# Performance work log

Hardware: AMD Instinct MI355X
Metric: run time of the kernel (lower is better)

## Reference

```python
import jax, jax.numpy as jnp
import numpy as np

B, D, U, M, K = 8192, 512, 512, 16, 64


def setup_inputs() -> dict:
    key = jax.random.key(0)
    ks = jax.random.split(key, 5)
    return {
        "x": jax.random.normal(ks[0], (B, D), dtype=jnp.float32),
        "key_kernel": jax.random.normal(ks[1], (D, K), dtype=jnp.float32) * (1.0 / np.sqrt(D)),
        "key_bias": jnp.zeros((K,), dtype=jnp.float32),
        "keys_map": jax.random.normal(ks[2], (M, K), dtype=jnp.float32),
        "kernels": jax.random.normal(ks[3], (M, D, U), dtype=jnp.float32) * (1.0 / np.sqrt(D)),
        "biases": jnp.zeros((M, U), dtype=jnp.float32),
    }


def reference(x, key_kernel, key_bias, keys_map, kernels, biases):
    # key projection: [B, K]
    keyv = x @ key_kernel + key_bias
    # inverse-distance similarity to mode keys: [B, M]
    dist = jnp.sqrt(jnp.sum((keyv[:, None, :] - keys_map[None, :, :]) ** 2, axis=-1))
    sim = 1.0 / (dist + 1.0)
    modes = kernels.shape[0]
    # kernel = mean_m(sim_m * kernels_m); out = x @ kernel.
    # Distributive identity: out = (1/M) * sum_m sim_m * (x @ kernels_m)
    out = jnp.einsum("bm,bd,mdu->bu", sim, x, kernels) / modes
    # bias = mean_m(sim_m * biases_m): [B, U]
    out = out + (sim @ biases) / modes
    return out
```

## Files before the change

### kernel.cpp

```cpp
#include <hip/hip_runtime.h>
#include <hip/hip_bf16.h>
#include <stdint.h>

#define B_SZ 8192
#define D_SZ 512
#define U_SZ 512
#define M_SZ 16
#define K_SZ 64

typedef short bf16x8 __attribute__((ext_vector_type(8)));
typedef float f32x4 __attribute__((ext_vector_type(4)));

__device__ __forceinline__ unsigned short f2bf(float f) {
  union { float f; unsigned u; } v; v.f = f;
  unsigned r = v.u + 0x7fffu + ((v.u >> 16) & 1u);
  return (unsigned short)(r >> 16);
}

__global__ __launch_bounds__(256) void prep1(
    const float* __restrict__ x, const float* __restrict__ key_kernel,
    const float* __restrict__ kernels, unsigned short* __restrict__ xbf,
    unsigned short* __restrict__ kbf, unsigned short* __restrict__ wkbf) {
  __shared__ float tf[32][65];
  __shared__ unsigned short sx[16][520];
  int bid = blockIdx.x;
  int t = threadIdx.x;

  if (bid < 2048) {
    int m = bid >> 7;
    int rem = bid & 127;
    int a = (rem >> 3) & 15;
    int ut = rem & 7;
    int d0 = a * 32, u0 = ut * 64;
    {
      int dr = t >> 4, uc = t & 15;
      const float* src = kernels + ((size_t)m * D_SZ + d0 + dr) * U_SZ + u0 + uc * 4;
      float4 aa = *(const float4*)src;
      float4 bb = *(const float4*)(src + (size_t)16 * U_SZ);
      tf[dr][uc * 4 + 0] = aa.x; tf[dr][uc * 4 + 1] = aa.y;
      tf[dr][uc * 4 + 2] = aa.z; tf[dr][uc * 4 + 3] = aa.w;
      tf[dr + 16][uc * 4 + 0] = bb.x; tf[dr + 16][uc * 4 + 1] = bb.y;
      tf[dr + 16][uc * 4 + 2] = bb.z; tf[dr + 16][uc * 4 + 3] = bb.w;
    }
    __syncthreads();
    {
      int ur = t >> 2, dc = t & 3;
      int j = ur >> 4, lane16 = ur & 15;
      int kt = a >> 1, h = a & 1;
      unsigned short* dst = kbf +
          (((((size_t)m * 8 + ut) * 8 + kt) * 4 + j) * 2 + h) * 512 +
          ((size_t)dc * 16 + lane16) * 8;
      ushort4 lo, hi;
      lo.x = f2bf(tf[dc * 8 + 0][ur]); lo.y = f2bf(tf[dc * 8 + 1][ur]);
      lo.z = f2bf(tf[dc * 8 + 2][ur]); lo.w = f2bf(tf[dc * 8 + 3][ur]);
      hi.x = f2bf(tf[dc * 8 + 4][ur]); hi.y = f2bf(tf[dc * 8 + 5][ur]);
      hi.z = f2bf(tf[dc * 8 + 6][ur]); hi.w = f2bf(tf[dc * 8 + 7][ur]);
      *(ushort4*)dst = lo;
      *(ushort4*)(dst + 4) = hi;
    }
    return;
  }

  if (bid < 2056) {
    int kt = bid - 2048;
#pragma unroll
    for (int rep = 0; rep < 2; ++rep) {
      int c = rep * 256 + t;
      int j = c >> 7, h = (c >> 6) & 1, quad = (c >> 4) & 3, ln = c & 15;
      int dd = kt * 64 + h * 32 + quad * 8;
      int u = j * 16 + ln;
      unsigned short v[8];
#pragma unroll
      for (int e = 0; e < 8; ++e)
        v[e] = f2bf(key_kernel[(size_t)(dd + e) * K_SZ + u]);
      unsigned short* dst =
          wkbf + ((size_t)((kt * 4 + j) * 2 + h) * 64 + quad * 16 + ln) * 8;
#pragma unroll
      for (int e = 0; e < 8; ++e) dst[e] = v[e];
    }
    return;
  }

  {
    int xb0 = bid - 2056;
    int btx = xb0 >> 3, i = xb0 & 7;
    int b0 = xb0 * 16;
#pragma unroll
    for (int rep = 0; rep < 8; ++rep) {
      int idx = rep * 256 + t;
      int row = idx >> 7;
      int c4 = (idx & 127) * 4;
      float4 v = *(const float4*)(x + (size_t)(b0 + row) * D_SZ + c4);
      ushort4 o;
      o.x = f2bf(v.x); o.y = f2bf(v.y); o.z = f2bf(v.z); o.w = f2bf(v.w);
      *(ushort4*)(&sx[row][c4]) = o;
    }
    __syncthreads();
    int w = t >> 6, l = t & 63;
    int ln = l & 15, quad = l >> 4;
#pragma unroll
    for (int rep = 0; rep < 4; ++rep) {
      int c = w * 4 + rep;
      int kt = c >> 1, h = c & 1;
      const unsigned short* srcp = &sx[ln][kt * 64 + h * 32 + quad * 8];
      ushort4 lo = *(const ushort4*)(srcp);
      ushort4 hi = *(const ushort4*)(srcp + 4);
      unsigned short* dst =
          xbf + ((((size_t)btx * 8 + kt) * 8 + i) * 2 + h) * 512 + (size_t)l * 8;
      *(ushort4*)dst = lo;
      *(ushort4*)(dst + 4) = hi;
    }
  }
}

__global__ __launch_bounds__(256) void prep2(
    const unsigned short* __restrict__ xbf, const unsigned short* __restrict__ wkbf,
    const float* __restrict__ key_bias, const float* __restrict__ keys_map,
    float* __restrict__ simT) {
  __shared__ float kv[64][68];
  __shared__ float sKM[16][64];
  int t = threadIdx.x, w = t >> 6, l = t & 63;
  int blk = blockIdx.x;
  int b0 = blk * 64, bt = blk >> 1, ibase = (blk & 1) * 4;
  int lane16 = l & 15, quad = l >> 4;

  ((float4*)sKM)[t] = ((const float4*)keys_map)[t];

  f32x4 acc[4];
#pragma unroll
  for (int j = 0; j < 4; ++j) acc[j] = (f32x4){0.f, 0.f, 0.f, 0.f};

  for (int kt = 0; kt < 8; ++kt) {
    bf16x8 af[2];
#pragma unroll
    for (int h = 0; h < 2; ++h)
      af[h] = *(const bf16x8*)(xbf +
                               ((((size_t)bt * 8 + kt) * 8 + ibase + w) * 2 + h) * 512 +
                               (size_t)l * 8);
#pragma unroll
    for (int j = 0; j < 4; ++j) {
      bf16x8 b0f = *(const bf16x8*)(wkbf + ((size_t)((kt * 4 + j) * 2 + 0) * 64 + l) * 8);
      bf16x8 b1f = *(const bf16x8*)(wkbf + ((size_t)((kt * 4 + j) * 2 + 1) * 64 + l) * 8);
      acc[j] = __builtin_amdgcn_mfma_f32_16x16x32_bf16(af[0], b0f, acc[j], 0, 0, 0);
      acc[j] = __builtin_amdgcn_mfma_f32_16x16x32_bf16(af[1], b1f, acc[j], 0, 0, 0);
    }
  }
#pragma unroll
  for (int j = 0; j < 4; ++j) {
    float bc = key_bias[j * 16 + lane16];
#pragma unroll
    for (int r = 0; r < 4; ++r)
      kv[w * 16 + quad * 4 + r][j * 16 + lane16] = acc[j][r] + bc;
  }
  __syncthreads();

  int row = t >> 2, mg = (t & 3) * 4;
  float d2[4] = {0.f, 0.f, 0.f, 0.f};
#pragma unroll 8
  for (int k = 0; k < 64; ++k) {
    float kvv = kv[row][k];
#pragma unroll
    for (int q = 0; q < 4; ++q) {
      float df = kvv - sKM[mg + q][k];
      d2[q] += df * df;
    }
  }
#pragma unroll
  for (int q = 0; q < 4; ++q)
    simT[(size_t)(mg + q) * B_SZ + b0 + row] = 1.0f / (sqrtf(d2[q]) + 1.0f);
}

#define STAGE(mode_, kt_, bufi_)                                               \
  {                                                                            \
    const unsigned short* _src = kbf_l +                                       \
        (((size_t)(mode_) * 8 + ut) * 8 + (kt_)) * 4096 + w * 1024;            \
    unsigned short* _dst = Bbuf + (bufi_) * 4096 + w * 1024;                   \
    __builtin_amdgcn_global_load_lds(                                          \
        (const __attribute__((address_space(1))) unsigned int*)(_src),         \
        (__attribute__((address_space(3))) unsigned int*)(_dst), 16, 0, 0);    \
    __builtin_amdgcn_global_load_lds(                                          \
        (const __attribute__((address_space(1))) unsigned int*)(_src + 512),   \
        (__attribute__((address_space(3))) unsigned int*)(_dst + 512), 16, 0,  \
        0);                                                                    \
  }

#define LOAD_AF(dst_, kt_)                                                     \
  _Pragma("unroll") for (int ii = 0; ii < 4; ++ii)                             \
      _Pragma("unroll") for (int h = 0; h < 2; ++h) dst_[ii][h] =              \
      *(const bf16x8*)(xbf +                                                   \
                       ((((size_t)(bt * 2 + (w >> 1)) * 8 + (kt_)) * 8 +       \
                         (w & 1) * 4 + ii) * 2 + h) * 512 +                    \
                       (size_t)l * 8);

__global__ __launch_bounds__(256, 1) void poly_gemm(
    const unsigned short* __restrict__ xbf,
    const unsigned short* __restrict__ kbf,
    const float* __restrict__ simT,
    const float* __restrict__ biases,
    float* __restrict__ out) {
  __shared__ __align__(16) char smem[53248];

  int t = threadIdx.x, w = t >> 6, l = t & 63;
  int bid = blockIdx.x;
  int ut = bid & 7, bt = bid >> 3;
  int b0 = bt * 256, u0 = ut * 64;
  int lane16 = l & 15, quad = l >> 4;

  unsigned short* Bbuf = (unsigned short*)smem;
  float* sSim = (float*)(smem + 32768);
  float* sBias = (float*)(smem + 49152);

  {
    int m = t >> 4, c = t & 15;
    const float* src = simT + (size_t)m * B_SZ + b0 + c * 16;
    float4* dst = (float4*)(sSim + m * 256 + c * 16);
#pragma unroll
    for (int q = 0; q < 4; ++q) dst[q] = ((const float4*)src)[q];
    *(float4*)(sBias + m * 64 + c * 4) =
        *(const float4*)(biases + (size_t)m * U_SZ + u0 + c * 4);
  }

  const unsigned short* kbf_l = kbf + (size_t)l * 8;

  bf16x8 afc[4][2], afn[4][2];

  STAGE(0, 0, 0);
  STAGE(1, 0, 1);
  LOAD_AF(afc, 0);
  asm volatile("s_waitcnt vmcnt(0)" ::: "memory");
  __syncthreads();

  f32x4 facc[4][4];
#pragma unroll
  for (int i = 0; i < 4; ++i)
#pragma unroll
    for (int j = 0; j < 4; ++j) facc[i][j] = (f32x4){0.f, 0.f, 0.f, 0.f};

#pragma unroll 1
  for (int kt = 0; kt < 8; ++kt) {
#pragma unroll 1
    for (int mg = 0; mg < 4; ++mg) {
#pragma unroll
      for (int mu = 0; mu < 4; ++mu) {
        const int mode = mg * 4 + mu;
        {
          int mode2 = (mode + 2) & 15;
          int kt2 = (mode >= 14) ? ((kt + 1) & 7) : kt;
          STAGE(mode2, kt2, (mode + 2) & 3);
        }
        if (mode == 0 && kt < 7) { LOAD_AF(afn, kt + 1); }
        if (mode <= 1 && kt <= 6)
          asm volatile("s_waitcnt vmcnt(12)" ::: "memory");
        else
          asm volatile("s_waitcnt vmcnt(4)" ::: "memory");
        asm volatile("s_barrier" ::: "memory");

        const unsigned short* lb = Bbuf + (mode & 3) * 4096;
        bf16x8 bfr[4][2];
#pragma unroll
        for (int j = 0; j < 4; ++j)
#pragma unroll
          for (int h = 0; h < 2; ++h)
            bfr[j][h] =
                *(const bf16x8*)(lb + (j * 2 + h) * 512 + (size_t)l * 8);

        f32x4 sv[4];
#pragma unroll
        for (int i = 0; i < 4; ++i)
          sv[i] = *(const f32x4*)(sSim + mode * 256 + w * 64 + i * 16 +
                                  quad * 4);

#pragma unroll
        for (int i = 0; i < 4; ++i)
#pragma unroll
          for (int j = 0; j < 4; ++j) {
            f32x4 p = __builtin_amdgcn_mfma_f32_16x16x32_bf16(
                afc[i][0], bfr[j][0], (f32x4){0.f, 0.f, 0.f, 0.f}, 0, 0, 0);
            p = __builtin_amdgcn_mfma_f32_16x16x32_bf16(afc[i][1], bfr[j][1],
                                                        p, 0, 0, 0);
#pragma unroll
            for (int r = 0; r < 4; ++r) facc[i][j][r] += sv[i][r] * p[r];
          }

        if (kt == 0) {
          float bbv[4];
#pragma unroll
          for (int j = 0; j < 4; ++j)
            bbv[j] = sBias[mode * 64 + j * 16 + lane16];
#pragma unroll
          for (int i = 0; i < 4; ++i)
#pragma unroll
            for (int j = 0; j < 4; ++j)
#pragma unroll
              for (int r = 0; r < 4; ++r)
                facc[i][j][r] += sv[i][r] * bbv[j];
        }
      }
    }
    if (kt < 7) {
#pragma unroll
      for (int ii = 0; ii < 4; ++ii)
#pragma unroll
        for (int h = 0; h < 2; ++h) afc[ii][h] = afn[ii][h];
    }
  }

  asm volatile("s_waitcnt vmcnt(0)" ::: "memory");
#pragma unroll
  for (int i = 0; i < 4; ++i)
#pragma unroll
    for (int r = 0; r < 4; ++r) {
      int row = b0 + w * 64 + i * 16 + quad * 4 + r;
      float* orow = out + (size_t)row * U_SZ + u0;
#pragma unroll
      for (int j = 0; j < 4; ++j)
        orow[j * 16 + lane16] = facc[i][j][r] * 0.0625f;
    }
}

extern "C" void kernel_launch(void* const* d_in, const int* in_sizes, int n_in,
                              void* d_out, int out_size, void* d_ws, size_t ws_size,
                              hipStream_t stream) {
  const float* x = (const float*)d_in[0];
  const float* key_kernel = (const float*)d_in[1];
  const float* key_bias = (const float*)d_in[2];
  const float* keys_map = (const float*)d_in[3];
  const float* kernels = (const float*)d_in[4];
  const float* biases = (const float*)d_in[5];
  float* out = (float*)d_out;

  char* p = (char*)d_ws;
  unsigned short* xbf = (unsigned short*)p;  p += (size_t)B_SZ * D_SZ * 2;
  unsigned short* kbf = (unsigned short*)p;  p += (size_t)M_SZ * U_SZ * D_SZ * 2;
  unsigned short* wkbf = (unsigned short*)p; p += (size_t)K_SZ * D_SZ * 2;
  float* simT = (float*)p;

  prep1<<<dim3(2568), 256, 0, stream>>>(x, key_kernel, kernels, xbf, kbf, wkbf);
  prep2<<<dim3(128), 256, 0, stream>>>(xbf, wkbf, key_bias, keys_map, simT);
  poly_gemm<<<dim3(256), 256, 0, stream>>>(xbf, kbf, simT, biases, out);
}
```

Measured before the change: 183.3 us.

## Use 8 waves per block with deeper 8-slot LDS weight pipeline

Doubles the poly_gemm block to 512 threads (8 waves). Each wave now owns 32 rows instead of 64, which halves the accumulator and A-fragment registers per wave. The LDS ring for weight tiles grows from 4 to 8 slots, prefetching 4 modes ahead instead of 2, and each wave stages half as much per step. The aim is more latency hiding through extra resident waves and a deeper prefetch. In exchange, LDS use rises to about 84KB and the launch-bounds hint of 2 blocks per CU may not be achievable, and the waitcnt accounting is more complex.

Result: faster. 163.4 us (-10.9%).

```diff
diff --git a/kernel.cpp b/kernel.cpp
--- a/kernel.cpp
+++ b/kernel.cpp
@@ -173,32 +173,30 @@
 #define STAGE(mode_, kt_, bufi_)                                               \
   {                                                                            \
     const unsigned short* _src = kbf_l +                                       \
-        (((size_t)(mode_) * 8 + ut) * 8 + (kt_)) * 4096 + w * 1024;            \
-    unsigned short* _dst = Bbuf + (bufi_) * 4096 + w * 1024;                   \
+        (((size_t)(mode_) * 8 + ut) * 8 + (kt_)) * 4096 + w * 512;             \
+    unsigned short* _dst = Bbuf + (bufi_) * 4096 + w * 512;                    \
     __builtin_amdgcn_global_load_lds(                                          \
         (const __attribute__((address_space(1))) unsigned int*)(_src),         \
         (__attribute__((address_space(3))) unsigned int*)(_dst), 16, 0, 0);    \
-    __builtin_amdgcn_global_load_lds(                                          \
-        (const __attribute__((address_space(1))) unsigned int*)(_src + 512),   \
-        (__attribute__((address_space(3))) unsigned int*)(_dst + 512), 16, 0,  \
-        0);                                                                    \
   }
 
 #define LOAD_AF(dst_, kt_)                                                     \
-  _Pragma("unroll") for (int ii = 0; ii < 4; ++ii)                             \
-      _Pragma("unroll") for (int h = 0; h < 2; ++h) dst_[ii][h] =              \
-      *(const bf16x8*)(xbf +                                                   \
-                       ((((size_t)(bt * 2 + (w >> 1)) * 8 + (kt_)) * 8 +       \
-                         (w & 1) * 4 + ii) * 2 + h) * 512 +                    \
-                       (size_t)l * 8);
-
-__global__ __launch_bounds__(256, 1) void poly_gemm(
+  _Pragma("unroll") for (int ii = 0; ii < 2; ++ii)                             \
+      _Pragma("unroll") for (int h = 0; h < 2; ++h) {                          \
+    int g_ = bt * 16 + w * 2 + ii;                                             \
+    dst_[ii][h] = *(const bf16x8*)(                                            \
+        xbf + ((((size_t)(g_ >> 3) * 8 + (kt_)) * 8 + (g_ & 7)) * 2 + h) *     \
+                  512 +                                                        \
+              (size_t)l * 8);                                                  \
+  }
+
+__global__ __launch_bounds__(512, 2) void poly_gemm(
     const unsigned short* __restrict__ xbf,
     const unsigned short* __restrict__ kbf,
     const float* __restrict__ simT,
     const float* __restrict__ biases,
     float* __restrict__ out) {
-  __shared__ __align__(16) char smem[53248];
+  __shared__ __align__(16) char smem[86016];
 
   int t = threadIdx.x, w = t >> 6, l = t & 63;
   int bid = blockIdx.x;
@@ -207,99 +205,101 @@
   int lane16 = l & 15, quad = l >> 4;
 
   unsigned short* Bbuf = (unsigned short*)smem;
-  float* sSim = (float*)(smem + 32768);
-  float* sBias = (float*)(smem + 49152);
+  float* sSim = (float*)(smem + 65536);
+  float* sBias = (float*)(smem + 81920);
 
   {
-    int m = t >> 4, c = t & 15;
-    const float* src = simT + (size_t)m * B_SZ + b0 + c * 16;
-    float4* dst = (float4*)(sSim + m * 256 + c * 16);
-#pragma unroll
-    for (int q = 0; q < 4; ++q) dst[q] = ((const float4*)src)[q];
-    *(float4*)(sBias + m * 64 + c * 4) =
-        *(const float4*)(biases + (size_t)m * U_SZ + u0 + c * 4);
+    int m = t >> 5, c = (t & 31) * 8;
+    const float* src = simT + (size_t)m * B_SZ + b0 + c;
+    float4* dst = (float4*)(sSim + m * 256 + c);
+    dst[0] = ((const float4*)src)[0];
+    dst[1] = ((const float4*)src)[1];
+    int bi = t * 2;
+    *(float2*)(sBias + bi) =
+        *(const float2*)(biases + (size_t)(bi >> 6) * U_SZ + u0 + (bi & 63));
   }
 
   const unsigned short* kbf_l = kbf + (size_t)l * 8;
 
-  bf16x8 afc[4][2], afn[4][2];
+  bf16x8 afc[2][2], afn[2][2];
 
   STAGE(0, 0, 0);
   STAGE(1, 0, 1);
+  STAGE(2, 0, 2);
+  STAGE(3, 0, 3);
   LOAD_AF(afc, 0);
   asm volatile("s_waitcnt vmcnt(0)" ::: "memory");
   __syncthreads();
 
-  f32x4 facc[4][4];
-#pragma unroll
-  for (int i = 0; i < 4; ++i)
+  f32x4 facc[2][4];
+#pragma unroll
+  for (int i = 0; i < 2; ++i)
 #pragma unroll
     for (int j = 0; j < 4; ++j) facc[i][j] = (f32x4){0.f, 0.f, 0.f, 0.f};
 
 #pragma unroll 1
   for (int kt = 0; kt < 8; ++kt) {
-#pragma unroll 1
-    for (int mg = 0; mg < 4; ++mg) {
-#pragma unroll
-      for (int mu = 0; mu < 4; ++mu) {
-        const int mode = mg * 4 + mu;
-        {
-          int mode2 = (mode + 2) & 15;
-          int kt2 = (mode >= 14) ? ((kt + 1) & 7) : kt;
-          STAGE(mode2, kt2, (mode + 2) & 3);
-        }
-        if (mode == 0 && kt < 7) { LOAD_AF(afn, kt + 1); }
-        if (mode <= 1 && kt <= 6)
-          asm volatile("s_waitcnt vmcnt(12)" ::: "memory");
+#pragma unroll
+    for (int mode = 0; mode < 16; ++mode) {
+      const int s = kt * 16 + mode;
+      {
+        int mode4 = (mode + 4) & 15;
+        int kt4 = (mode >= 12) ? ((kt + 1) & 7) : kt;
+        STAGE(mode4, kt4, (s + 4) & 7);
+      }
+      if (mode == 0 && kt < 7) { LOAD_AF(afn, kt + 1); }
+      if (mode < 5) {
+        if (kt < 7)
+          asm volatile("s_waitcnt vmcnt(8)" ::: "memory");
         else
           asm volatile("s_waitcnt vmcnt(4)" ::: "memory");
-        asm volatile("s_barrier" ::: "memory");
-
-        const unsigned short* lb = Bbuf + (mode & 3) * 4096;
-        bf16x8 bfr[4][2];
+      } else {
+        asm volatile("s_waitcnt vmcnt(4)" ::: "memory");
+      }
+      asm volatile("s_barrier" ::: "memory");
+
+      const unsigned short* lb = Bbuf + (s & 7) * 4096;
+      bf16x8 bfr[4][2];
+#pragma unroll
+      for (int j = 0; j < 4; ++j)
+#pragma unroll
+        for (int h = 0; h < 2; ++h)
+          bfr[j][h] = *(const bf16x8*)(lb + (j * 2 + h) * 512 + (size_t)l * 8);
+
+      f32x4 sv[2];
+#pragma unroll
+      for (int i = 0; i < 2; ++i)
+        sv[i] =
+            *(const f32x4*)(sSim + mode * 256 + w * 32 + i * 16 + quad * 4);
+
+#pragma unroll
+      for (int i = 0; i < 2; ++i)
+#pragma unroll
+        for (int j = 0; j < 4; ++j) {
+          f32x4 p = __builtin_amdgcn_mfma_f32_16x16x32_bf16(
+              afc[i][0], bfr[j][0], (f32x4){0.f, 0.f, 0.f, 0.f}, 0, 0, 0);
+          p = __builtin_amdgcn_mfma_f32_16x16x32_bf16(afc[i][1], bfr[j][1], p,
+                                                      0, 0, 0);
+#pragma unroll
+          for (int r = 0; r < 4; ++r) facc[i][j][r] += sv[i][r] * p[r];
+        }
+
+      if (kt == 0) {
+        float bbv[4];
 #pragma unroll
         for (int j = 0; j < 4; ++j)
-#pragma unroll
-          for (int h = 0; h < 2; ++h)
-            bfr[j][h] =
-                *(const bf16x8*)(lb + (j * 2 + h) * 512 + (size_t)l * 8);
-
-        f32x4 sv[4];
-#pragma unroll
-        for (int i = 0; i < 4; ++i)
-          sv[i] = *(const f32x4*)(sSim + mode * 256 + w * 64 + i * 16 +
-                                  quad * 4);
-
-#pragma unroll
-        for (int i = 0; i < 4; ++i)
-#pragma unroll
-          for (int j = 0; j < 4; ++j) {
-            f32x4 p = __builtin_amdgcn_mfma_f32_16x16x32_bf16(
-                afc[i][0], bfr[j][0], (f32x4){0.f, 0.f, 0.f, 0.f}, 0, 0, 0);
-            p = __builtin_amdgcn_mfma_f32_16x16x32_bf16(afc[i][1], bfr[j][1],
-                                                        p, 0, 0, 0);
-#pragma unroll
-            for (int r = 0; r < 4; ++r) facc[i][j][r] += sv[i][r] * p[r];
-          }
-
-        if (kt == 0) {
-          float bbv[4];
+          bbv[j] = sBias[mode * 64 + j * 16 + lane16];
+#pragma unroll
+        for (int i = 0; i < 2; ++i)
 #pragma unroll
           for (int j = 0; j < 4; ++j)
-            bbv[j] = sBias[mode * 64 + j * 16 + lane16];
-#pragma unroll
-          for (int i = 0; i < 4; ++i)
-#pragma unroll
-            for (int j = 0; j < 4; ++j)
-#pragma unroll
-              for (int r = 0; r < 4; ++r)
-                facc[i][j][r] += sv[i][r] * bbv[j];
-        }
+#pragma unroll
+            for (int r = 0; r < 4; ++r) facc[i][j][r] += sv[i][r] * bbv[j];
       }
     }
     if (kt < 7) {
 #pragma unroll
-      for (int ii = 0; ii < 4; ++ii)
+      for (int ii = 0; ii < 2; ++ii)
 #pragma unroll
         for (int h = 0; h < 2; ++h) afc[ii][h] = afn[ii][h];
     }
@@ -307,10 +307,10 @@
 
   asm volatile("s_waitcnt vmcnt(0)" ::: "memory");
 #pragma unroll
-  for (int i = 0; i < 4; ++i)
+  for (int i = 0; i < 2; ++i)
 #pragma unroll
     for (int r = 0; r < 4; ++r) {
-      int row = b0 + w * 64 + i * 16 + quad * 4 + r;
+      int row = b0 + w * 32 + i * 16 + quad * 4 + r;
       float* orow = out + (size_t)row * U_SZ + u0;
 #pragma unroll
       for (int j = 0; j < 4; ++j)
@@ -337,5 +337,5 @@
 
   prep1<<<dim3(2568), 256, 0, stream>>>(x, key_kernel, kernels, xbf, kbf, wkbf);
   prep2<<<dim3(128), 256, 0, stream>>>(xbf, wkbf, key_bias, keys_map, simT);
-  poly_gemm<<<dim3(256), 256, 0, stream>>>(xbf, kbf, simT, biases, out);
-}
+  poly_gemm<<<dim3(256), 512, 0, stream>>>(xbf, kbf, simT, biases, out);
+}
```
